# Kernel tuning notes

Hardware: AMD Instinct MI355X
Metric: run time of the kernel (lower is better)

## Reference

```python
import jax, jax.numpy as jnp
import numpy as np

D_MODEL = 1024
NUM_HEADS = 16
DEPTH = D_MODEL // NUM_HEADS


def setup_inputs() -> dict:
    key = jax.random.key(0)
    ks = jax.random.split(key, 9)
    B, S = 2, 2048
    s = 1.0 / np.sqrt(D_MODEL)
    return {
        "x": jax.random.normal(ks[0], (B, S, D_MODEL), dtype=jnp.float32),
        "wq": jax.random.normal(ks[1], (D_MODEL, D_MODEL), dtype=jnp.float32) * s,
        "bq": jnp.zeros((D_MODEL,), dtype=jnp.float32),
        "wk": jax.random.normal(ks[2], (D_MODEL, D_MODEL), dtype=jnp.float32) * s,
        "bk": jnp.zeros((D_MODEL,), dtype=jnp.float32),
        "wv": jax.random.normal(ks[3], (D_MODEL, D_MODEL), dtype=jnp.float32) * s,
        "bv": jnp.zeros((D_MODEL,), dtype=jnp.float32),
        "wo": jax.random.normal(ks[4], (D_MODEL, D_MODEL), dtype=jnp.float32) * s,
        "bo": jnp.zeros((D_MODEL,), dtype=jnp.float32),
    }


def _split_heads(t):
    # [B, S, D] -> [B, H, S, depth]
    B, S, _ = t.shape
    return t.reshape(B, S, NUM_HEADS, DEPTH).transpose(0, 2, 1, 3)


def reference(x, wq, bq, wk, bk, wv, bv, wo, bo):
    B, S, _ = x.shape
    q = _split_heads(x @ wq + bq)
    k = _split_heads(x @ wk + bk)
    v = _split_heads(x @ wv + bv)
    scale = 1.0 / jnp.sqrt(jnp.asarray(DEPTH, dtype=x.dtype))
    logits = jnp.einsum("bhsd,bhtd->bhst", q, k) * scale  # [B,H,S,S]
    attn = jax.nn.softmax(logits, axis=-1)
    ctx = jnp.einsum("bhst,bhtd->bhsd", attn, v)  # [B,H,S,depth]
    concat = ctx.transpose(0, 2, 1, 3).reshape(B, S, D_MODEL)
    return concat @ wo + bo
```

## Files before the change

### kernel.cpp

```cpp
#include <hip/hip_runtime.h>
#include <hip/hip_bf16.h>

typedef __bf16 bf16;
typedef __bf16 bf16x4 __attribute__((ext_vector_type(4)));
typedef __bf16 bf16x8 __attribute__((ext_vector_type(8)));
typedef float f32x4 __attribute__((ext_vector_type(4)));

typedef __attribute__((address_space(3))) void lds_void;
typedef const __attribute__((address_space(1))) void gbl_void;

#define D_MODEL 1024
#define NHEAD 16
#define DEPTH 64
#define SEQ 2048
#define BATCH 2
#define NTOK (BATCH * SEQ)
#define ROWS (BATCH * NHEAD * SEQ)

#define Q_SCALE 0.18033688f

__global__ __launch_bounds__(256) void convert_f32_bf16(const float* __restrict__ src,
                                                        bf16* __restrict__ dst) {
    int i = blockIdx.x * 256 + threadIdx.x;
    float4 v = ((const float4*)src)[i];
    bf16x4 o = {(bf16)v.x, (bf16)v.y, (bf16)v.z, (bf16)v.w};
    *(bf16x4*)&dst[(size_t)i * 4] = o;
}

__global__ __launch_bounds__(256) void transpose_convert(const float* __restrict__ w0,
                                                         const float* __restrict__ w1,
                                                         const float* __restrict__ w2,
                                                         const float* __restrict__ w3,
                                                         bf16* __restrict__ dst) {
    int z = blockIdx.z;
    const float* w = (z == 0) ? w0 : (z == 1) ? w1 : (z == 2) ? w2 : w3;
    bf16* d = dst + (size_t)z * D_MODEL * D_MODEL;
    __shared__ float tile[32][33];
    int c0 = blockIdx.x * 32;
    int r0 = blockIdx.y * 32;
    int tx = threadIdx.x, ty = threadIdx.y;
#pragma unroll
    for (int i = 0; i < 4; i++)
        tile[ty + i * 8][tx] = w[(size_t)(r0 + ty + i * 8) * D_MODEL + c0 + tx];
    __syncthreads();
#pragma unroll
    for (int i = 0; i < 4; i++)
        d[(size_t)(c0 + ty + i * 8) * D_MODEL + r0 + tx] = (bf16)tile[tx][ty + i * 8];
}

template <bool SWAP>
__device__ __forceinline__ void gemm_core(const bf16* __restrict__ A,
                                          const bf16* __restrict__ Bt,
                                          int row0, int col0,
                                          bf16* As, bf16* Bs, f32x4 acc[4][4]) {
    const int tid = threadIdx.x;
    const int lane = tid & 63, wave = tid >> 6;
    const int quad = lane >> 4, l16 = lane & 15;
    const int wm = (wave & 1) << 6, wn = (wave >> 1) << 6;
    const int srow = lane >> 2, selem = (lane & 3) * 8;

    for (int k0 = 0; k0 < D_MODEL; k0 += 32) {
        __syncthreads();
#pragma unroll
        for (int t = 0; t < 2; t++) {
            int m = wave * 2 + t;
            const bf16* ga = A + (size_t)(row0 + m * 16 + srow) * D_MODEL + k0 + selem;
            const bf16* gb = Bt + (size_t)(col0 + m * 16 + srow) * D_MODEL + k0 + selem;
            __builtin_amdgcn_global_load_lds((gbl_void*)ga, (lds_void*)(As + m * 512 + lane * 8), 16, 0, 0);
            __builtin_amdgcn_global_load_lds((gbl_void*)gb, (lds_void*)(Bs + m * 512 + lane * 8), 16, 0, 0);
        }
        __syncthreads();
        bf16x8 af[4], bfr[4];
#pragma unroll
        for (int i = 0; i < 4; i++)
            af[i] = *(const bf16x8*)&As[(wm + i * 16 + l16) * 32 + quad * 8];
#pragma unroll
        for (int j = 0; j < 4; j++)
            bfr[j] = *(const bf16x8*)&Bs[(wn + j * 16 + l16) * 32 + quad * 8];
#pragma unroll
        for (int i = 0; i < 4; i++)
#pragma unroll
            for (int j = 0; j < 4; j++)
                acc[i][j] = SWAP
                    ? __builtin_amdgcn_mfma_f32_16x16x32_bf16(bfr[j], af[i], acc[i][j], 0, 0, 0)
                    : __builtin_amdgcn_mfma_f32_16x16x32_bf16(af[i], bfr[j], acc[i][j], 0, 0, 0);
    }
}

__global__ __launch_bounds__(256) void qkv_gemm(const bf16* __restrict__ xb,
                                                const bf16* __restrict__ wtb,
                                                const float* __restrict__ bq,
                                                const float* __restrict__ bk,
                                                const float* __restrict__ bv,
                                                bf16* __restrict__ q,
                                                bf16* __restrict__ k,
                                                bf16* __restrict__ v) {
    __shared__ bf16 As[128 * 32];
    __shared__ bf16 Bs[128 * 32];
    int z = blockIdx.z;
    const bf16* Bt = wtb + (size_t)z * D_MODEL * D_MODEL;
    const float* bias = (z == 0) ? bq : (z == 1) ? bk : bv;
    int row0 = blockIdx.y * 128, col0 = blockIdx.x * 128;
    f32x4 acc[4][4] = {};

    const int lane = threadIdx.x & 63, wave = threadIdx.x >> 6;
    const int quad = lane >> 4, l16 = lane & 15;
    const int wm = (wave & 1) << 6, wn = (wave >> 1) << 6;

    if (z < 2) {
        gemm_core<false>(xb, Bt, row0, col0, As, Bs, acc);
        bf16* dst = (z == 0) ? q : k;
        const float sc = (z == 0) ? Q_SCALE : 1.0f;
#pragma unroll
        for (int i = 0; i < 4; i++) {
#pragma unroll
            for (int j = 0; j < 4; j++) {
                int colg = col0 + wn + j * 16 + l16;
                int hh = colg >> 6, d = colg & 63;
                float bi = bias[colg];
                int rbase = row0 + wm + i * 16 + quad * 4;
                int b = rbase >> 11, sb = rbase & 2047;
#pragma unroll
                for (int r = 0; r < 4; r++) {
                    size_t idx = ((size_t)(b * NHEAD + hh) * SEQ + sb + r) * DEPTH + d;
                    dst[idx] = (bf16)((acc[i][j][r] + bi) * sc);
                }
            }
        }
    } else {
        gemm_core<true>(xb, Bt, row0, col0, As, Bs, acc);
#pragma unroll
        for (int i = 0; i < 4; i++) {
            int tok = row0 + wm + i * 16 + l16;
            int b = tok >> 11, sb = tok & 2047;
#pragma unroll
            for (int j = 0; j < 4; j++) {
#pragma unroll
                for (int r = 0; r < 4; r++) {
                    int f = col0 + wn + j * 16 + quad * 4 + r;
                    int hh = f >> 6, d = f & 63;
                    v[((size_t)(b * NHEAD + hh) * DEPTH + d) * SEQ + sb] =
                        (bf16)(acc[i][j][r] + bias[f]);
                }
            }
        }
    }
}

__global__ __launch_bounds__(256) void attn(const bf16* __restrict__ q,
                                            const bf16* __restrict__ k,
                                            const bf16* __restrict__ v,
                                            bf16* __restrict__ ctx,
                                            float* __restrict__ ovp,
                                            float* __restrict__ lp,
                                            int kv_chunk) {
    __shared__ bf16 Ks[64 * 72];
    __shared__ bf16 Vs[64 * 72];
    __shared__ bf16 Ps[4][32 * 72];
    const int tid = threadIdx.x;
    const int lane = tid & 63, wave = tid >> 6;
    const int quad = lane >> 4, l16 = lane & 15;
    const int bh = blockIdx.y;
    const int q0 = blockIdx.x * 128;
    const int kv0 = blockIdx.z * kv_chunk;
    const int kv_end = kv0 + kv_chunk;
    const size_t hb = (size_t)bh * SEQ * DEPTH;
    const bf16* qh = q + hb;
    const bf16* kh = k + hb;
    const bf16* vh = v + hb;

    bf16x8 bq_[2][2];
#pragma unroll
    for (int g = 0; g < 2; g++) {
        int qrow = q0 + wave * 32 + g * 16 + l16;
#pragma unroll
        for (int c = 0; c < 2; c++)
            bq_[g][c] = *(const bf16x8*)&qh[(size_t)qrow * DEPTH + c * 32 + quad * 8];
    }
    bf16* myP = &Ps[wave][0];

    bf16x8 ones;
#pragma unroll
    for (int i = 0; i < 8; i++) ones[i] = (bf16)1.0f;

    f32x4 ov[2][4] = {};
    f32x4 lacc[2] = {};

    const int srow = tid >> 2, scol = (tid & 3) << 4;
    const bf16* kg = kh + (size_t)srow * DEPTH + scol;
    const bf16* vg = vh + (size_t)srow * SEQ + scol;
    bf16* ksd = &Ks[srow * 72 + scol];
    bf16* vsd = &Vs[srow * 72 + scol];

    bf16x8 kr0 = *(const bf16x8*)(kg + (size_t)kv0 * DEPTH);
    bf16x8 kr1 = *(const bf16x8*)(kg + (size_t)kv0 * DEPTH + 8);
    bf16x8 vr0 = *(const bf16x8*)(vg + kv0);
    bf16x8 vr1 = *(const bf16x8*)(vg + kv0 + 8);

    for (int t0 = kv0; t0 < kv_end; t0 += 64) {
        __syncthreads();
        *(bf16x8*)ksd = kr0;  *(bf16x8*)(ksd + 8) = kr1;
        *(bf16x8*)vsd = vr0;  *(bf16x8*)(vsd + 8) = vr1;
        __syncthreads();
        if (t0 + 64 < kv_end) {
            const bf16* kgn = kg + (size_t)(t0 + 64) * DEPTH;
            const bf16* vgn = vg + (t0 + 64);
            kr0 = *(const bf16x8*)kgn;  kr1 = *(const bf16x8*)(kgn + 8);
            vr0 = *(const bf16x8*)vgn;  vr1 = *(const bf16x8*)(vgn + 8);
        }
        f32x4 sc[2][4] = {};
#pragma unroll
        for (int c = 0; c < 2; c++)
#pragma unroll
            for (int j = 0; j < 4; j++) {
                bf16x8 kf = *(const bf16x8*)&Ks[(j * 16 + l16) * 72 + c * 32 + quad * 8];
#pragma unroll
                for (int g = 0; g < 2; g++)
                    sc[g][j] = __builtin_amdgcn_mfma_f32_16x16x32_bf16(kf, bq_[g][c], sc[g][j], 0, 0, 0);
            }
#pragma unroll
        for (int g = 0; g < 2; g++)
#pragma unroll
            for (int j = 0; j < 4; j++) {
                bf16x4 pb = {(bf16)__builtin_amdgcn_exp2f(sc[g][j][0]),
                             (bf16)__builtin_amdgcn_exp2f(sc[g][j][1]),
                             (bf16)__builtin_amdgcn_exp2f(sc[g][j][2]),
                             (bf16)__builtin_amdgcn_exp2f(sc[g][j][3])};
                *(bf16x4*)&myP[(g * 16 + l16) * 72 + j * 16 + quad * 4] = pb;
            }
#pragma unroll
        for (int c = 0; c < 2; c++) {
            bf16x8 pf[2];
#pragma unroll
            for (int g = 0; g < 2; g++) {
                pf[g] = *(const bf16x8*)&myP[(g * 16 + l16) * 72 + c * 32 + quad * 8];
                lacc[g] = __builtin_amdgcn_mfma_f32_16x16x32_bf16(ones, pf[g], lacc[g], 0, 0, 0);
            }
#pragma unroll
            for (int t = 0; t < 4; t++) {
                bf16x8 vf = *(const bf16x8*)&Vs[(t * 16 + l16) * 72 + c * 32 + quad * 8];
#pragma unroll
                for (int g = 0; g < 2; g++)
                    ov[g][t] = __builtin_amdgcn_mfma_f32_16x16x32_bf16(vf, pf[g], ov[g][t], 0, 0, 0);
            }
        }
    }
    if (ovp) {
        size_t zb = (size_t)blockIdx.z * ROWS;
#pragma unroll
        for (int g = 0; g < 2; g++) {
            int s = q0 + wave * 32 + g * 16 + l16;
            size_t row = zb + (size_t)bh * SEQ + s;
#pragma unroll
            for (int t = 0; t < 4; t++)
                *(f32x4*)&ovp[row * DEPTH + t * 16 + quad * 4] = ov[g][t];
            if (quad == 0) lp[row] = lacc[g][0];
        }
    } else {
        int b = bh >> 4, hh = bh & 15;
#pragma unroll
        for (int g = 0; g < 2; g++) {
            float inv = 1.0f / lacc[g][0];
            size_t rowb = ((size_t)(b * SEQ + q0 + wave * 32 + g * 16 + l16)) * D_MODEL + hh * 64;
#pragma unroll
            for (int t = 0; t < 4; t++) {
                bf16x4 ob = {(bf16)(ov[g][t][0] * inv), (bf16)(ov[g][t][1] * inv),
                             (bf16)(ov[g][t][2] * inv), (bf16)(ov[g][t][3] * inv)};
                *(bf16x4*)&ctx[rowb + t * 16 + quad * 4] = ob;
            }
        }
    }
}

__global__ __launch_bounds__(256) void reduce_ctx(const float* __restrict__ ovp,
                                                  const float* __restrict__ lp,
                                                  bf16* __restrict__ ctx,
                                                  int ksplit) {
    int idx = blockIdx.x * 256 + threadIdx.x;
    int d4 = idx & 15;
    size_t row = (size_t)(idx >> 4);
    f32x4 o = {};
    float l = 0.f;
    for (int z = 0; z < ksplit; z++) {
        o += *(const f32x4*)&ovp[((size_t)z * ROWS + row) * DEPTH + d4 * 4];
        l += lp[(size_t)z * ROWS + row];
    }
    float inv = 1.0f / l;
    int bh = (int)(row >> 11);
    int s = (int)(row & 2047);
    int b = bh >> 4, hh = bh & 15;
    bf16x4 ob = {(bf16)(o[0] * inv), (bf16)(o[1] * inv),
                 (bf16)(o[2] * inv), (bf16)(o[3] * inv)};
    *(bf16x4*)&ctx[((size_t)(b * SEQ + s)) * D_MODEL + hh * 64 + d4 * 4] = ob;
}

__global__ __launch_bounds__(256) void out_gemm(const bf16* __restrict__ ctx,
                                                const bf16* __restrict__ wot,
                                                const float* __restrict__ bo,
                                                float* __restrict__ out) {
    __shared__ bf16 As[128 * 32];
    __shared__ bf16 Bs[128 * 32];
    int row0 = blockIdx.y * 128, col0 = blockIdx.x * 128;
    f32x4 acc[4][4] = {};
    gemm_core<false>(ctx, wot, row0, col0, As, Bs, acc);

    const int lane = threadIdx.x & 63, wave = threadIdx.x >> 6;
    const int quad = lane >> 4, l16 = lane & 15;
    const int wm = (wave & 1) << 6, wn = (wave >> 1) << 6;
#pragma unroll
    for (int i = 0; i < 4; i++)
#pragma unroll
        for (int j = 0; j < 4; j++) {
            int colg = col0 + wn + j * 16 + l16;
            float bi = bo[colg];
            int rbase = row0 + wm + i * 16 + quad * 4;
#pragma unroll
            for (int r = 0; r < 4; r++)
                out[(size_t)(rbase + r) * D_MODEL + colg] = acc[i][j][r] + bi;
        }
}

extern "C" void kernel_launch(void* const* d_in, const int* in_sizes, int n_in,
                              void* d_out, int out_size, void* d_ws, size_t ws_size,
                              hipStream_t stream) {
    const float* x  = (const float*)d_in[0];
    const float* wq = (const float*)d_in[1];
    const float* bq = (const float*)d_in[2];
    const float* wk = (const float*)d_in[3];
    const float* bk = (const float*)d_in[4];
    const float* wv = (const float*)d_in[5];
    const float* bv = (const float*)d_in[6];
    const float* wo = (const float*)d_in[7];
    const float* bo = (const float*)d_in[8];
    float* out = (float*)d_out;

    const size_t MB = 1024 * 1024;
    char* ws = (char*)d_ws;
    bf16* xb  = (bf16*)(ws);
    bf16* wtb = (bf16*)(ws + 8 * MB);
    bf16* qb  = (bf16*)(ws + 16 * MB);
    bf16* kb  = (bf16*)(ws + 24 * MB);
    bf16* vb  = (bf16*)(ws + 32 * MB);
    bf16* ctx = (bf16*)(ws + 40 * MB);
    float* ovp = (float*)(ws + 48 * MB);
    float* lp  = (float*)(ws + 82 * MB);

    const int ksplit = (ws_size >= 84 * MB) ? 2 : 0;

    convert_f32_bf16<<<NTOK * D_MODEL / 1024, 256, 0, stream>>>(x, xb);
    transpose_convert<<<dim3(32, 32, 4), dim3(32, 8), 0, stream>>>(wq, wk, wv, wo, wtb);
    qkv_gemm<<<dim3(8, 32, 3), 256, 0, stream>>>(xb, wtb, bq, bk, bv, qb, kb, vb);
    if (ksplit == 2) {
        attn<<<dim3(SEQ / 128, BATCH * NHEAD, 2), 256, 0, stream>>>(
            qb, kb, vb, ctx, ovp, lp, SEQ / 2);
        reduce_ctx<<<ROWS * 16 / 256, 256, 0, stream>>>(ovp, lp, ctx, 2);
    } else {
        attn<<<dim3(SEQ / 128, BATCH * NHEAD, 1), 256, 0, stream>>>(
            qb, kb, vb, ctx, nullptr, nullptr, SEQ);
    }
    out_gemm<<<dim3(8, 32), 256, 0, stream>>>(ctx, wtb + 3 * (size_t)D_MODEL * D_MODEL, bo, out);
}
```

Measured before the change: 224.0 us.

## Drop split-KV attention for double-buffered async-LDS single pass with swizzled tiles

Attention now runs as one pass over the full sequence, which removes the fp32 partial-output workspace and the separate reduce kernel. Each block shrinks to two waves, and each wave handles 64 query rows, so every K/V tile is reused across more queries. K/V tiles are copied straight into double-buffered LDS with global_load_lds, so the next tile arrives while the current one is computed. An XOR swizzle replaces the padded layout to avoid bank conflicts. The cost is fewer waves per CU and higher register pressure, which may limit latency hiding.

```diff
diff --git a/kernel.cpp b/kernel.cpp
--- a/kernel.cpp
+++ b/kernel.cpp
@@ -15,7 +15,6 @@
 #define SEQ 2048
 #define BATCH 2
 #define NTOK (BATCH * SEQ)
-#define ROWS (BATCH * NHEAD * SEQ)
 
 #define Q_SCALE 0.18033688f
 
@@ -147,32 +146,29 @@
     }
 }
 
-__global__ __launch_bounds__(256) void attn(const bf16* __restrict__ q,
-                                            const bf16* __restrict__ k,
-                                            const bf16* __restrict__ v,
-                                            bf16* __restrict__ ctx,
-                                            float* __restrict__ ovp,
-                                            float* __restrict__ lp,
-                                            int kv_chunk) {
-    __shared__ bf16 Ks[64 * 72];
-    __shared__ bf16 Vs[64 * 72];
-    __shared__ bf16 Ps[4][32 * 72];
+#define KVFRAG(buf, R, CH) (*(const bf16x8*)&(buf)[(size_t)(R) * 64 + (((CH) ^ ((R) & 7)) << 3)])
+
+__global__ __launch_bounds__(128, 2) void attn(const bf16* __restrict__ q,
+                                               const bf16* __restrict__ k,
+                                               const bf16* __restrict__ v,
+                                               bf16* __restrict__ ctx) {
+    __shared__ bf16 Ks[2][64 * 64];
+    __shared__ bf16 Vs[2][64 * 64];
+    __shared__ bf16 Ps[2][64 * 72];
     const int tid = threadIdx.x;
     const int lane = tid & 63, wave = tid >> 6;
     const int quad = lane >> 4, l16 = lane & 15;
     const int bh = blockIdx.y;
     const int q0 = blockIdx.x * 128;
-    const int kv0 = blockIdx.z * kv_chunk;
-    const int kv_end = kv0 + kv_chunk;
     const size_t hb = (size_t)bh * SEQ * DEPTH;
     const bf16* qh = q + hb;
     const bf16* kh = k + hb;
     const bf16* vh = v + hb;
 
-    bf16x8 bq_[2][2];
-#pragma unroll
-    for (int g = 0; g < 2; g++) {
-        int qrow = q0 + wave * 32 + g * 16 + l16;
+    bf16x8 bq_[4][2];
+#pragma unroll
+    for (int g = 0; g < 4; g++) {
+        int qrow = q0 + wave * 64 + g * 16 + l16;
 #pragma unroll
         for (int c = 0; c < 2; c++)
             bq_[g][c] = *(const bf16x8*)&qh[(size_t)qrow * DEPTH + c * 32 + quad * 8];
@@ -183,43 +179,53 @@
 #pragma unroll
     for (int i = 0; i < 8; i++) ones[i] = (bf16)1.0f;
 
-    f32x4 ov[2][4] = {};
-    f32x4 lacc[2] = {};
-
-    const int srow = tid >> 2, scol = (tid & 3) << 4;
-    const bf16* kg = kh + (size_t)srow * DEPTH + scol;
-    const bf16* vg = vh + (size_t)srow * SEQ + scol;
-    bf16* ksd = &Ks[srow * 72 + scol];
-    bf16* vsd = &Vs[srow * 72 + scol];
-
-    bf16x8 kr0 = *(const bf16x8*)(kg + (size_t)kv0 * DEPTH);
-    bf16x8 kr1 = *(const bf16x8*)(kg + (size_t)kv0 * DEPTH + 8);
-    bf16x8 vr0 = *(const bf16x8*)(vg + kv0);
-    bf16x8 vr1 = *(const bf16x8*)(vg + kv0 + 8);
-
-    for (int t0 = kv0; t0 < kv_end; t0 += 64) {
+    f32x4 ov[4][4] = {};
+    f32x4 lacc[4] = {};
+
+    const int srow8 = lane >> 3;
+    const int sch = (lane & 7) ^ srow8;
+
+#pragma unroll
+    for (int R = 0; R < 4; R++) {
+        int rows8 = R * 2 + wave;
+        int r = rows8 * 8 + srow8;
+        __builtin_amdgcn_global_load_lds((gbl_void*)(kh + (size_t)r * DEPTH + sch * 8),
+                                         (lds_void*)(&Ks[0][0] + rows8 * 512 + lane * 8), 16, 0, 0);
+        __builtin_amdgcn_global_load_lds((gbl_void*)(vh + (size_t)r * SEQ + sch * 8),
+                                         (lds_void*)(&Vs[0][0] + rows8 * 512 + lane * 8), 16, 0, 0);
+    }
+
+    for (int it = 0; it < SEQ / 64; it++) {
+        const int cur = it & 1;
         __syncthreads();
-        *(bf16x8*)ksd = kr0;  *(bf16x8*)(ksd + 8) = kr1;
-        *(bf16x8*)vsd = vr0;  *(bf16x8*)(vsd + 8) = vr1;
-        __syncthreads();
-        if (t0 + 64 < kv_end) {
-            const bf16* kgn = kg + (size_t)(t0 + 64) * DEPTH;
-            const bf16* vgn = vg + (t0 + 64);
-            kr0 = *(const bf16x8*)kgn;  kr1 = *(const bf16x8*)(kgn + 8);
-            vr0 = *(const bf16x8*)vgn;  vr1 = *(const bf16x8*)(vgn + 8);
-        }
-        f32x4 sc[2][4] = {};
+        if (it + 1 < SEQ / 64) {
+            const int nxt = cur ^ 1;
+            int t1 = (it + 1) * 64;
+#pragma unroll
+            for (int R = 0; R < 4; R++) {
+                int rows8 = R * 2 + wave;
+                int r = rows8 * 8 + srow8;
+                __builtin_amdgcn_global_load_lds((gbl_void*)(kh + (size_t)(t1 + r) * DEPTH + sch * 8),
+                                                 (lds_void*)(&Ks[nxt][0] + rows8 * 512 + lane * 8), 16, 0, 0);
+                __builtin_amdgcn_global_load_lds((gbl_void*)(vh + (size_t)r * SEQ + t1 + sch * 8),
+                                                 (lds_void*)(&Vs[nxt][0] + rows8 * 512 + lane * 8), 16, 0, 0);
+            }
+        }
+        const bf16* Kc = &Ks[cur][0];
+        const bf16* Vc = &Vs[cur][0];
+
+        f32x4 sc[4][4] = {};
 #pragma unroll
         for (int c = 0; c < 2; c++)
 #pragma unroll
             for (int j = 0; j < 4; j++) {
-                bf16x8 kf = *(const bf16x8*)&Ks[(j * 16 + l16) * 72 + c * 32 + quad * 8];
-#pragma unroll
-                for (int g = 0; g < 2; g++)
+                bf16x8 kf = KVFRAG(Kc, j * 16 + l16, c * 4 + quad);
+#pragma unroll
+                for (int g = 0; g < 4; g++)
                     sc[g][j] = __builtin_amdgcn_mfma_f32_16x16x32_bf16(kf, bq_[g][c], sc[g][j], 0, 0, 0);
             }
 #pragma unroll
-        for (int g = 0; g < 2; g++)
+        for (int g = 0; g < 4; g++)
 #pragma unroll
             for (int j = 0; j < 4; j++) {
                 bf16x4 pb = {(bf16)__builtin_amdgcn_exp2f(sc[g][j][0]),
@@ -230,68 +236,33 @@
             }
 #pragma unroll
         for (int c = 0; c < 2; c++) {
-            bf16x8 pf[2];
-#pragma unroll
-            for (int g = 0; g < 2; g++) {
+            bf16x8 pf[4];
+#pragma unroll
+            for (int g = 0; g < 4; g++) {
                 pf[g] = *(const bf16x8*)&myP[(g * 16 + l16) * 72 + c * 32 + quad * 8];
                 lacc[g] = __builtin_amdgcn_mfma_f32_16x16x32_bf16(ones, pf[g], lacc[g], 0, 0, 0);
             }
 #pragma unroll
             for (int t = 0; t < 4; t++) {
-                bf16x8 vf = *(const bf16x8*)&Vs[(t * 16 + l16) * 72 + c * 32 + quad * 8];
-#pragma unroll
-                for (int g = 0; g < 2; g++)
+                bf16x8 vf = KVFRAG(Vc, t * 16 + l16, c * 4 + quad);
+#pragma unroll
+                for (int g = 0; g < 4; g++)
                     ov[g][t] = __builtin_amdgcn_mfma_f32_16x16x32_bf16(vf, pf[g], ov[g][t], 0, 0, 0);
             }
         }
     }
-    if (ovp) {
-        size_t zb = (size_t)blockIdx.z * ROWS;
-#pragma unroll
-        for (int g = 0; g < 2; g++) {
-            int s = q0 + wave * 32 + g * 16 + l16;
-            size_t row = zb + (size_t)bh * SEQ + s;
-#pragma unroll
-            for (int t = 0; t < 4; t++)
-                *(f32x4*)&ovp[row * DEPTH + t * 16 + quad * 4] = ov[g][t];
-            if (quad == 0) lp[row] = lacc[g][0];
-        }
-    } else {
-        int b = bh >> 4, hh = bh & 15;
-#pragma unroll
-        for (int g = 0; g < 2; g++) {
-            float inv = 1.0f / lacc[g][0];
-            size_t rowb = ((size_t)(b * SEQ + q0 + wave * 32 + g * 16 + l16)) * D_MODEL + hh * 64;
-#pragma unroll
-            for (int t = 0; t < 4; t++) {
-                bf16x4 ob = {(bf16)(ov[g][t][0] * inv), (bf16)(ov[g][t][1] * inv),
-                             (bf16)(ov[g][t][2] * inv), (bf16)(ov[g][t][3] * inv)};
-                *(bf16x4*)&ctx[rowb + t * 16 + quad * 4] = ob;
-            }
-        }
-    }
-}
-
-__global__ __launch_bounds__(256) void reduce_ctx(const float* __restrict__ ovp,
-                                                  const float* __restrict__ lp,
-                                                  bf16* __restrict__ ctx,
-                                                  int ksplit) {
-    int idx = blockIdx.x * 256 + threadIdx.x;
-    int d4 = idx & 15;
-    size_t row = (size_t)(idx >> 4);
-    f32x4 o = {};
-    float l = 0.f;
-    for (int z = 0; z < ksplit; z++) {
-        o += *(const f32x4*)&ovp[((size_t)z * ROWS + row) * DEPTH + d4 * 4];
-        l += lp[(size_t)z * ROWS + row];
-    }
-    float inv = 1.0f / l;
-    int bh = (int)(row >> 11);
-    int s = (int)(row & 2047);
     int b = bh >> 4, hh = bh & 15;
-    bf16x4 ob = {(bf16)(o[0] * inv), (bf16)(o[1] * inv),
-                 (bf16)(o[2] * inv), (bf16)(o[3] * inv)};
-    *(bf16x4*)&ctx[((size_t)(b * SEQ + s)) * D_MODEL + hh * 64 + d4 * 4] = ob;
+#pragma unroll
+    for (int g = 0; g < 4; g++) {
+        float inv = 1.0f / lacc[g][0];
+        size_t rowb = ((size_t)(b * SEQ + q0 + wave * 64 + g * 16 + l16)) * D_MODEL + hh * 64;
+#pragma unroll
+        for (int t = 0; t < 4; t++) {
+            bf16x4 ob = {(bf16)(ov[g][t][0] * inv), (bf16)(ov[g][t][1] * inv),
+                         (bf16)(ov[g][t][2] * inv), (bf16)(ov[g][t][3] * inv)};
+            *(bf16x4*)&ctx[rowb + t * 16 + quad * 4] = ob;
+        }
+    }
 }
 
 __global__ __launch_bounds__(256) void out_gemm(const bf16* __restrict__ ctx,
@@ -342,21 +313,10 @@
     bf16* kb  = (bf16*)(ws + 24 * MB);
     bf16* vb  = (bf16*)(ws + 32 * MB);
     bf16* ctx = (bf16*)(ws + 40 * MB);
-    float* ovp = (float*)(ws + 48 * MB);
-    float* lp  = (float*)(ws + 82 * MB);
-
-    const int ksplit = (ws_size >= 84 * MB) ? 2 : 0;
 
     convert_f32_bf16<<<NTOK * D_MODEL / 1024, 256, 0, stream>>>(x, xb);
     transpose_convert<<<dim3(32, 32, 4), dim3(32, 8), 0, stream>>>(wq, wk, wv, wo, wtb);
     qkv_gemm<<<dim3(8, 32, 3), 256, 0, stream>>>(xb, wtb, bq, bk, bv, qb, kb, vb);
-    if (ksplit == 2) {
-        attn<<<dim3(SEQ / 128, BATCH * NHEAD, 2), 256, 0, stream>>>(
-            qb, kb, vb, ctx, ovp, lp, SEQ / 2);
-        reduce_ctx<<<ROWS * 16 / 256, 256, 0, stream>>>(ovp, lp, ctx, 2);
-    } else {
-        attn<<<dim3(SEQ / 128, BATCH * NHEAD, 1), 256, 0, stream>>>(
-            qb, kb, vb, ctx, nullptr, nullptr, SEQ);
-    }
+    attn<<<dim3(SEQ / 128, BATCH * NHEAD), 128, 0, stream>>>(qb, kb, vb, ctx);
     out_gemm<<<dim3(8, 32), 256, 0, stream>>>(ctx, wtb + 3 * (size_t)D_MODEL * D_MODEL, bo, out);
 }
```

After: 230.6 us. +2.9%, slower.
